# Optimization experiments

Measured on AMD Instinct MI355X. Metric: run time of the kernel, lower is better.

Reference implementation:

```python
import jax, jax.numpy as jnp
import numpy as np

TEMPERATURE = 0.07
EPS = 1e-12  # F.normalize eps


def setup_inputs() -> dict:
    key = jax.random.key(0)
    k1, k2 = jax.random.split(key)
    B, D = 4096, 1024
    return {
        "features_1": jax.random.normal(k1, (B, D), dtype=jnp.float32),
        "features_2": jax.random.normal(k2, (B, D), dtype=jnp.float32),
    }


def _l2_normalize(x):
    n = jnp.sqrt(jnp.sum(x * x, axis=1, keepdims=True))
    return x / jnp.maximum(n, EPS)


def reference(features_1, features_2):
    B = features_1.shape[0]
    f1 = _l2_normalize(features_1)
    f2 = _l2_normalize(features_2)
    f = jnp.concatenate([f1, f2], axis=0)  # [2B, D]
    # cosine sim of already-normalized vectors == plain matmul
    sim = (f @ f.T) / TEMPERATURE  # [2B, 2B]
    # denominator: logsumexp over each row excluding the diagonal (self-sim)
    eye = jnp.eye(2 * B, dtype=bool)
    lse = jax.nn.logsumexp(jnp.where(eye, -jnp.inf, sim), axis=1)  # [2B]
    # positives: cross-view pairs (i+B, i) then (i, i+B)
    idx = jnp.arange(B)
    pos = jnp.concatenate([sim[idx + B, idx], sim[idx, idx + B]], axis=0)  # [2B]
    loss = -jnp.mean(pos - lse)
    return loss
```

## Files before the change

### kernel.cpp

```cpp
#include <hip/hip_runtime.h>
#include <hip/hip_bf16.h>
#include <math.h>

#define INV_T (1.0f / 0.07f)

typedef __bf16 bf16x8 __attribute__((ext_vector_type(8)));
typedef float f32x4 __attribute__((ext_vector_type(4)));

__device__ __forceinline__ void gld16(const void* g, void* l) {
    __builtin_amdgcn_global_load_lds(
        (const __attribute__((address_space(1))) unsigned int*)g,
        (__attribute__((address_space(3))) unsigned int*)l,
        16, 0, 0);
}

__device__ __forceinline__ float agent_load(const float* p) {
    return __hip_atomic_load(p, __ATOMIC_RELAXED, __HIP_MEMORY_SCOPE_AGENT);
}

__global__ __launch_bounds__(256) void norm_kernel(
    const float4* __restrict__ f1, const float4* __restrict__ f2,
    ushort4* __restrict__ F, float* __restrict__ S, float* __restrict__ P,
    int* __restrict__ cnt, int B) {
    const int i = blockIdx.x;
    const int t = threadIdx.x;

    float4 x = f1[i * 256 + t];
    float4 y = f2[i * 256 + t];

    float s1 = x.x * x.x + x.y * x.y + x.z * x.z + x.w * x.w;
    float s2 = y.x * y.x + y.y * y.y + y.z * y.z + y.w * y.w;
    float dd = x.x * y.x + x.y * y.y + x.z * y.z + x.w * y.w;

    for (int o = 32; o > 0; o >>= 1) {
        s1 += __shfl_down(s1, o);
        s2 += __shfl_down(s2, o);
        dd += __shfl_down(dd, o);
    }
    __shared__ float red[4][3];
    const int wv = t >> 6, ln = t & 63;
    if (ln == 0) { red[wv][0] = s1; red[wv][1] = s2; red[wv][2] = dd; }
    __syncthreads();
    s1 = red[0][0] + red[1][0] + red[2][0] + red[3][0];
    s2 = red[0][1] + red[1][1] + red[2][1] + red[3][1];
    dd = red[0][2] + red[1][2] + red[2][2] + red[3][2];

    const float rn1 = 1.0f / fmaxf(sqrtf(s1), 1e-12f);
    const float rn2 = 1.0f / fmaxf(sqrtf(s2), 1e-12f);

    union { ushort4 u; __hip_bfloat16 h[4]; } p;
    p.h[0] = __float2bfloat16(x.x * rn1);
    p.h[1] = __float2bfloat16(x.y * rn1);
    p.h[2] = __float2bfloat16(x.z * rn1);
    p.h[3] = __float2bfloat16(x.w * rn1);
    F[(size_t)i * 256 + t] = p.u;
    p.h[0] = __float2bfloat16(y.x * rn2);
    p.h[1] = __float2bfloat16(y.y * rn2);
    p.h[2] = __float2bfloat16(y.z * rn2);
    p.h[3] = __float2bfloat16(y.w * rn2);
    F[(size_t)(B + i) * 256 + t] = p.u;

    if (t == 0) {
        P[i] = dd * rn1 * rn2;
        S[i] = 0.0f;
        S[B + i] = 0.0f;
        if (i == 0) { cnt[0] = 0; cnt[1] = 0; }
    }
}

__global__ __launch_bounds__(256, 2) void sim_kernel(
    const __hip_bfloat16* __restrict__ F, float* __restrict__ S,
    const float* __restrict__ P, float* __restrict__ out,
    int* __restrict__ cnt, int N, int B, int D, int ntiles) {
    __shared__ __align__(16) __hip_bfloat16 smem[16384];
    __hip_bfloat16 (*As)[64] = (__hip_bfloat16(*)[64])smem;
    __hip_bfloat16 (*Bs)[64] = (__hip_bfloat16(*)[64])(smem + 8192);
    int* kSh = (int*)smem;
    int* lastF = ((int*)smem) + 1;
    float (*redf)[2] = (float(*)[2])(smem + 16);

    const int tid  = threadIdx.x;
    const int wave = tid >> 6;
    const int lane = tid & 63;
    const int quad = lane >> 4;
    const int l16  = lane & 15;

    const int srow   = lane >> 3;
    const int ldsOff = (lane & 7) * 8;
    const int srcOff = ((lane & 7) ^ srow) * 8;

    const int waveRow = (wave >> 1) * 64;
    const int waveCol = (wave & 1) * 64;
    const int swz = l16 & 7;

    for (;;) {
        if (tid == 0) *kSh = atomicAdd(&cnt[0], 1);
        __syncthreads();
        const int k = *kSh;
        __syncthreads();
        if (k >= ntiles) break;

        int tjj = (int)((sqrtf(8.0f * (float)k + 1.0f) - 1.0f) * 0.5f);
        while ((tjj + 1) * (tjj + 2) / 2 <= k) ++tjj;
        while (tjj * (tjj + 1) / 2 > k) --tjj;
        const int tii = k - tjj * (tjj + 1) / 2;
        const int bRow = tii * 128;
        const int bCol = tjj * 128;

        f32x4 acc[4][4];
#pragma unroll
        for (int mi = 0; mi < 4; ++mi)
#pragma unroll
            for (int ni = 0; ni < 4; ++ni)
                acc[mi][ni] = (f32x4){0.0f, 0.0f, 0.0f, 0.0f};

        for (int kb = 0; kb < D; kb += 64) {
#pragma unroll
            for (int p = 0; p < 4; ++p) {
                const int rowT = (p * 4 + wave) * 8 + srow;
                gld16(&F[(size_t)(bRow + rowT) * D + kb + srcOff], &As[rowT][ldsOff]);
            }
#pragma unroll
            for (int p = 0; p < 4; ++p) {
                const int rowT = (p * 4 + wave) * 8 + srow;
                gld16(&F[(size_t)(bCol + rowT) * D + kb + srcOff], &Bs[rowT][ldsOff]);
            }
            __syncthreads();

#pragma unroll
            for (int ks = 0; ks < 2; ++ks) {
                const int slot = ((ks * 4 + quad) ^ swz) * 8;
                bf16x8 bf[4];
#pragma unroll
                for (int ni = 0; ni < 4; ++ni)
                    bf[ni] = *(const bf16x8*)&Bs[waveCol + ni * 16 + l16][slot];
#pragma unroll
                for (int mi = 0; mi < 4; ++mi) {
                    const bf16x8 af = *(const bf16x8*)&As[waveRow + mi * 16 + l16][slot];
#pragma unroll
                    for (int ni = 0; ni < 4; ++ni)
                        acc[mi][ni] = __builtin_amdgcn_mfma_f32_16x16x32_bf16(
                            af, bf[ni], acc[mi][ni], 0, 0, 0);
                }
            }
            __syncthreads();
        }

#pragma unroll
        for (int mi = 0; mi < 4; ++mi)
#pragma unroll
            for (int ni = 0; ni < 4; ++ni)
#pragma unroll
                for (int r = 0; r < 4; ++r) {
                    const int gRow = bRow + waveRow + mi * 16 + quad * 4 + r;
                    const int gCol = bCol + waveCol + ni * 16 + l16;
                    acc[mi][ni][r] = (gRow < gCol)
                        ? __expf((acc[mi][ni][r] - 1.0f) * INV_T) : 0.0f;
                }

#pragma unroll
        for (int mi = 0; mi < 4; ++mi)
#pragma unroll
            for (int r = 0; r < 4; ++r) {
                const int gRow = bRow + waveRow + mi * 16 + quad * 4 + r;
                float v = acc[mi][0][r] + acc[mi][1][r] + acc[mi][2][r] + acc[mi][3][r];
                v += __shfl_xor(v, 1);
                v += __shfl_xor(v, 2);
                v += __shfl_xor(v, 4);
                v += __shfl_xor(v, 8);
                if (l16 == 0) atomicAdd(&S[gRow], v);
            }

#pragma unroll
        for (int ni = 0; ni < 4; ++ni) {
            float cv = 0.0f;
#pragma unroll
            for (int mi = 0; mi < 4; ++mi)
#pragma unroll
                for (int r = 0; r < 4; ++r) cv += acc[mi][ni][r];
            cv += __shfl_xor(cv, 16);
            cv += __shfl_xor(cv, 32);
            if (quad == 0) atomicAdd(&S[bCol + waveCol + ni * 16 + l16], cv);
        }
    }

    asm volatile("s_waitcnt vmcnt(0) lgkmcnt(0)" ::: "memory");
    if (tid == 0) *lastF = (atomicAdd(&cnt[1], 1) == (int)gridDim.x - 1);
    __syncthreads();
    if (!*lastF) return;

    float s0 = 0.0f, s1 = 0.0f, s2 = 0.0f, s3 = 0.0f;
    for (int i = tid; i < N; i += 1024) {
        const float a = agent_load(&S[i]);
        const float b = agent_load(&S[i + 256]);
        const float c = agent_load(&S[i + 512]);
        const float d = agent_load(&S[i + 768]);
        s0 += __logf(a); s1 += __logf(b); s2 += __logf(c); s3 += __logf(d);
    }
    float s = (s0 + s1) + (s2 + s3);

    float pp = 0.0f;
    for (int i = tid; i < B; i += 1024)
        pp += P[i] + P[i + 256] + P[i + 512] + P[i + 768];

    for (int o = 32; o > 0; o >>= 1) {
        s += __shfl_down(s, o);
        pp += __shfl_down(pp, o);
    }
    if (lane == 0) { redf[wave][0] = s; redf[wave][1] = pp; }
    __syncthreads();
    if (tid == 0) {
        const float sl = redf[0][0] + redf[1][0] + redf[2][0] + redf[3][0];
        const float ps = redf[0][1] + redf[1][1] + redf[2][1] + redf[3][1];
        out[0] = INV_T + sl / (float)N - ps * (2.0f * INV_T / (float)N);
    }
}

extern "C" void kernel_launch(void* const* d_in, const int* in_sizes, int n_in,
                              void* d_out, int out_size, void* d_ws, size_t ws_size,
                              hipStream_t stream) {
    const int D = 1024;
    const int B = in_sizes[0] / D;
    const int N = 2 * B;
    const int M = N / 128;
    const int ntiles = M * (M + 1) / 2;
    const int nblocks = 1280;

    const float* f1 = (const float*)d_in[0];
    const float* f2 = (const float*)d_in[1];

    __hip_bfloat16* F = (__hip_bfloat16*)d_ws;
    float* S = (float*)((char*)d_ws + (size_t)N * D * sizeof(__hip_bfloat16));
    float* P = S + N;
    int* cnt = (int*)(P + B);

    norm_kernel<<<dim3(B), dim3(256), 0, stream>>>(
        (const float4*)f1, (const float4*)f2, (ushort4*)F, S, P, cnt, B);
    sim_kernel<<<dim3(nblocks), dim3(256), 0, stream>>>(
        F, S, P, (float*)d_out, cnt, N, B, D, ntiles);
}
```

Baseline: 185.8 us.

## Schedule off-diagonal tiles first and skip redundant work on diagonal tiles

The tile order is changed so that all strictly off-diagonal tiles are handed out first and the 64 diagonal tiles come last. For diagonal tiles only one operand is loaded into LDS and reused for both sides. The wave covering the fully masked lower sub-block skips its MFMAs and epilogue, and the mixed wave issues only the upper-triangular MFMA sub-tiles. The persistent grid also shrinks from 1280 to 1024 blocks. This removes redundant global loads and matrix work on diagonal tiles, but leaves waves unevenly loaded within a diagonal tile and adds per-tile branching.

```diff
diff --git a/kernel.cpp b/kernel.cpp
--- a/kernel.cpp
+++ b/kernel.cpp
@@ -71,7 +71,7 @@
 __global__ __launch_bounds__(256, 2) void sim_kernel(
     const __hip_bfloat16* __restrict__ F, float* __restrict__ S,
     const float* __restrict__ P, float* __restrict__ out,
-    int* __restrict__ cnt, int N, int B, int D, int ntiles) {
+    int* __restrict__ cnt, int N, int B, int D, int noff, int ntiles) {
     __shared__ __align__(16) __hip_bfloat16 smem[16384];
     __hip_bfloat16 (*As)[64] = (__hip_bfloat16(*)[64])smem;
     __hip_bfloat16 (*Bs)[64] = (__hip_bfloat16(*)[64])(smem + 8192);
@@ -100,19 +100,32 @@
         __syncthreads();
         if (k >= ntiles) break;
 
-        int tjj = (int)((sqrtf(8.0f * (float)k + 1.0f) - 1.0f) * 0.5f);
-        while ((tjj + 1) * (tjj + 2) / 2 <= k) ++tjj;
-        while (tjj * (tjj + 1) / 2 > k) --tjj;
-        const int tii = k - tjj * (tjj + 1) / 2;
+        int tii, tjj;
+        if (k < noff) {
+            tjj = (int)((1.0f + sqrtf(8.0f * (float)k + 1.0f)) * 0.5f);
+            while (tjj * (tjj - 1) / 2 > k) --tjj;
+            while ((tjj + 1) * tjj / 2 <= k) ++tjj;
+            tii = k - tjj * (tjj - 1) / 2;
+        } else {
+            tii = tjj = k - noff;
+        }
+        const bool isDiag = (tii == tjj);
         const int bRow = tii * 128;
         const int bCol = tjj * 128;
 
+        const bool fullMfma = !isDiag || (wave == 1);
+        const bool skipMfma = isDiag && (wave == 2);
+
         f32x4 acc[4][4];
 #pragma unroll
         for (int mi = 0; mi < 4; ++mi)
 #pragma unroll
             for (int ni = 0; ni < 4; ++ni)
                 acc[mi][ni] = (f32x4){0.0f, 0.0f, 0.0f, 0.0f};
+
+        const __hip_bfloat16 (*Bsrc)[64] =
+            isDiag ? (const __hip_bfloat16(*)[64])As
+                   : (const __hip_bfloat16(*)[64])Bs;
 
         for (int kb = 0; kb < D; kb += 64) {
 #pragma unroll
@@ -120,67 +133,85 @@
                 const int rowT = (p * 4 + wave) * 8 + srow;
                 gld16(&F[(size_t)(bRow + rowT) * D + kb + srcOff], &As[rowT][ldsOff]);
             }
-#pragma unroll
-            for (int p = 0; p < 4; ++p) {
-                const int rowT = (p * 4 + wave) * 8 + srow;
-                gld16(&F[(size_t)(bCol + rowT) * D + kb + srcOff], &Bs[rowT][ldsOff]);
+            if (!isDiag) {
+#pragma unroll
+                for (int p = 0; p < 4; ++p) {
+                    const int rowT = (p * 4 + wave) * 8 + srow;
+                    gld16(&F[(size_t)(bCol + rowT) * D + kb + srcOff], &Bs[rowT][ldsOff]);
+                }
             }
             __syncthreads();
 
-#pragma unroll
-            for (int ks = 0; ks < 2; ++ks) {
-                const int slot = ((ks * 4 + quad) ^ swz) * 8;
-                bf16x8 bf[4];
-#pragma unroll
-                for (int ni = 0; ni < 4; ++ni)
-                    bf[ni] = *(const bf16x8*)&Bs[waveCol + ni * 16 + l16][slot];
-#pragma unroll
-                for (int mi = 0; mi < 4; ++mi) {
-                    const bf16x8 af = *(const bf16x8*)&As[waveRow + mi * 16 + l16][slot];
+            if (!skipMfma) {
+#pragma unroll
+                for (int ks = 0; ks < 2; ++ks) {
+                    const int slot = ((ks * 4 + quad) ^ swz) * 8;
+                    bf16x8 bf[4];
 #pragma unroll
                     for (int ni = 0; ni < 4; ++ni)
-                        acc[mi][ni] = __builtin_amdgcn_mfma_f32_16x16x32_bf16(
-                            af, bf[ni], acc[mi][ni], 0, 0, 0);
+                        bf[ni] = *(const bf16x8*)&Bsrc[waveCol + ni * 16 + l16][slot];
+                    if (fullMfma) {
+#pragma unroll
+                        for (int mi = 0; mi < 4; ++mi) {
+                            const bf16x8 af = *(const bf16x8*)&As[waveRow + mi * 16 + l16][slot];
+#pragma unroll
+                            for (int ni = 0; ni < 4; ++ni)
+                                acc[mi][ni] = __builtin_amdgcn_mfma_f32_16x16x32_bf16(
+                                    af, bf[ni], acc[mi][ni], 0, 0, 0);
+                        }
+                    } else {
+#pragma unroll
+                        for (int mi = 0; mi < 4; ++mi) {
+                            const bf16x8 af = *(const bf16x8*)&As[waveRow + mi * 16 + l16][slot];
+#pragma unroll
+                            for (int ni = 0; ni < 4; ++ni)
+                                if (ni >= mi)
+                                    acc[mi][ni] = __builtin_amdgcn_mfma_f32_16x16x32_bf16(
+                                        af, bf[ni], acc[mi][ni], 0, 0, 0);
+                        }
+                    }
                 }
             }
             __syncthreads();
         }
 
-#pragma unroll
-        for (int mi = 0; mi < 4; ++mi)
-#pragma unroll
-            for (int ni = 0; ni < 4; ++ni)
+        if (!skipMfma) {
+#pragma unroll
+            for (int mi = 0; mi < 4; ++mi)
+#pragma unroll
+                for (int ni = 0; ni < 4; ++ni)
+#pragma unroll
+                    for (int r = 0; r < 4; ++r) {
+                        const int gRow = bRow + waveRow + mi * 16 + quad * 4 + r;
+                        const int gCol = bCol + waveCol + ni * 16 + l16;
+                        acc[mi][ni][r] = (gRow < gCol)
+                            ? __expf((acc[mi][ni][r] - 1.0f) * INV_T) : 0.0f;
+                    }
+
+#pragma unroll
+            for (int mi = 0; mi < 4; ++mi)
 #pragma unroll
                 for (int r = 0; r < 4; ++r) {
                     const int gRow = bRow + waveRow + mi * 16 + quad * 4 + r;
-                    const int gCol = bCol + waveCol + ni * 16 + l16;
-                    acc[mi][ni][r] = (gRow < gCol)
-                        ? __expf((acc[mi][ni][r] - 1.0f) * INV_T) : 0.0f;
+                    float v = acc[mi][0][r] + acc[mi][1][r] + acc[mi][2][r] + acc[mi][3][r];
+                    v += __shfl_xor(v, 1);
+                    v += __shfl_xor(v, 2);
+                    v += __shfl_xor(v, 4);
+                    v += __shfl_xor(v, 8);
+                    if (l16 == 0) atomicAdd(&S[gRow], v);
                 }
 
 #pragma unroll
-        for (int mi = 0; mi < 4; ++mi)
-#pragma unroll
-            for (int r = 0; r < 4; ++r) {
-                const int gRow = bRow + waveRow + mi * 16 + quad * 4 + r;
-                float v = acc[mi][0][r] + acc[mi][1][r] + acc[mi][2][r] + acc[mi][3][r];
-                v += __shfl_xor(v, 1);
-                v += __shfl_xor(v, 2);
-                v += __shfl_xor(v, 4);
-                v += __shfl_xor(v, 8);
-                if (l16 == 0) atomicAdd(&S[gRow], v);
-            }
-
-#pragma unroll
-        for (int ni = 0; ni < 4; ++ni) {
-            float cv = 0.0f;
-#pragma unroll
-            for (int mi = 0; mi < 4; ++mi)
-#pragma unroll
-                for (int r = 0; r < 4; ++r) cv += acc[mi][ni][r];
-            cv += __shfl_xor(cv, 16);
-            cv += __shfl_xor(cv, 32);
-            if (quad == 0) atomicAdd(&S[bCol + waveCol + ni * 16 + l16], cv);
+            for (int ni = 0; ni < 4; ++ni) {
+                float cv = 0.0f;
+#pragma unroll
+                for (int mi = 0; mi < 4; ++mi)
+#pragma unroll
+                    for (int r = 0; r < 4; ++r) cv += acc[mi][ni][r];
+                cv += __shfl_xor(cv, 16);
+                cv += __shfl_xor(cv, 32);
+                if (quad == 0) atomicAdd(&S[bCol + waveCol + ni * 16 + l16], cv);
+            }
         }
     }
 
@@ -223,8 +254,9 @@
     const int B = in_sizes[0] / D;
     const int N = 2 * B;
     const int M = N / 128;
-    const int ntiles = M * (M + 1) / 2;
-    const int nblocks = 1280;
+    const int noff = M * (M - 1) / 2;
+    const int ntiles = noff + M;
+    const int nblocks = 1024;
 
     const float* f1 = (const float*)d_in[0];
     const float* f2 = (const float*)d_in[1];
@@ -237,5 +269,5 @@
     norm_kernel<<<dim3(B), dim3(256), 0, stream>>>(
         (const float4*)f1, (const float4*)f2, (ushort4*)F, S, P, cnt, B);
     sim_kernel<<<dim3(nblocks), dim3(256), 0, stream>>>(
-        F, S, P, (float*)d_out, cnt, N, B, D, ntiles);
-}
+        F, S, P, (float*)d_out, cnt, N, B, D, noff, ntiles);
+}
```

New measurement: 196.7 us. 5.9% more time.
